# Performance work log

Hardware: AMD Instinct MI355X
Metric: run time of the kernel (lower is better)

Reference implementation:

```python
import jax, jax.numpy as jnp
import numpy as np

NUM_HEADS = 8
HEAD_DIM = 64
SCALE = HEAD_DIM ** -0.5
EPS = 1e-5
STRIDE = (2, 2)


def _layernorm(x, g, b):
    mu = x.mean(-1, keepdims=True)
    var = x.var(-1, keepdims=True)
    return (x - mu) * jax.lax.rsqrt(var + EPS) * g + b


def _pool(t, convw, ln_g, ln_b, H):
    # t: (B, T, nh, 1 + H*H, d); depthwise-conv pool of spatial tokens, cls kept as-is,
    # LayerNorm over per-head channel dim applied after re-attaching cls (matches torch).
    B, T, nh, N, d = t.shape
    t = t.reshape(B * T, nh, N, d)
    cls_tok, body = t[:, :, :1], t[:, :, 1:]
    xs = body.reshape(B * T * nh, H, H, d)
    xs = jax.lax.conv_general_dilated(
        xs, convw, window_strides=STRIDE, padding=((1, 1), (1, 1)),
        dimension_numbers=('NHWC', 'HWIO', 'NHWC'), feature_group_count=d)
    Ho, Wo = xs.shape[1], xs.shape[2]
    xs = xs.reshape(B * T, nh, Ho * Wo, d)
    xs = jnp.concatenate([cls_tok, xs], axis=2)
    xs = _layernorm(xs, ln_g, ln_b)
    return xs.reshape(B, T, nh, Ho * Wo + 1, d), (Ho, Wo)


def _lin(t, w, b):
    # (B, T, nh, n, d) -> fold heads -> Linear(nh*d -> nh*d) -> unfold heads
    B, T, nh, n, d = t.shape
    y = t.transpose(0, 1, 3, 2, 4).reshape(B * T, n, nh * d)
    y = y @ w.T + b
    return y.reshape(B, T, n, nh, d).transpose(0, 1, 3, 2, 4)


def reference(x, x_ref, w_q, b_q, w_k, b_k, w_v, b_v, w_proj, b_proj,
              convw_q, convw_k, convw_v, ln_g_q, ln_b_q, ln_g_k, ln_b_k,
              ln_g_v, ln_b_v, rel_pos_h, rel_pos_w, hw_shape):
    B, T1, N, C = x.shape
    T2 = x_ref.shape[1]
    nh, d = NUM_HEADS, C // NUM_HEADS
    H = int(hw_shape)
    # pool_first: split heads before pooling;  q from x, k = v from x_ref
    q = x.reshape(B, T1, N, nh, d).transpose(0, 1, 3, 2, 4)
    kv = x_ref.reshape(B, T2, N, nh, d).transpose(0, 1, 3, 2, 4)
    q, q_shape = _pool(q, convw_q, ln_g_q, ln_b_q, H)
    k, k_shape = _pool(kv, convw_k, ln_g_k, ln_b_k, H)
    v, _ = _pool(kv, convw_v, ln_g_v, ln_b_v, H)
    q = _lin(q, w_q, b_q)
    k = _lin(k, w_k, b_k)
    v = _lin(v, w_v, b_v)
    # b t nh n d -> b nh (t n) d
    q = q.transpose(0, 2, 1, 3, 4).reshape(B, nh, -1, d)
    k = k.transpose(0, 2, 1, 3, 4).reshape(B, nh, -1, d)
    v = v.transpose(0, 2, 1, 3, 4).reshape(B, nh, -1, d)
    attn = jnp.einsum('bhqd,bhkd->bhqk', q * SCALE, k)
    # inline spatial relative position bias (uses UNSCALED q, as in torch source)
    qh, qw = q_shape
    kh, kw = k_shape
    dh = (np.arange(qh)[:, None] * max(kh / qh, 1.0)
          - np.arange(kh)[None, :] * max(qh / kh, 1.0)
          + (kh - 1) * max(qh / kh, 1.0)).astype(np.int32)
    dw = (np.arange(qw)[:, None] * max(kw / qw, 1.0)
          - np.arange(kw)[None, :] * max(qw / kw, 1.0)
          + (kw - 1) * max(qw / kw, 1.0)).astype(np.int32)
    Rh = rel_pos_h[dh]  # (qh, kh, d)
    Rw = rel_pos_w[dw]  # (qw, kw, d)
    r_q = q[:, :, 1:].reshape(B, nh, qh, qw, d)
    rel_h = jnp.einsum('byhwc,hkc->byhwk', r_q, Rh)
    rel_w = jnp.einsum('byhwc,wkc->byhwk', r_q, Rw)
    bias = (rel_h[..., :, None] + rel_w[..., None, :]).reshape(B, nh, qh * qw, kh * kw)
    attn = attn.at[:, :, 1:, 1:].add(bias)
    attn = jax.nn.softmax(attn, axis=-1)
    out = jnp.einsum('bhqk,bhkd->bhqd', attn, v)
    # residual pooling (skips cls token)
    out = out.at[:, :, 1:, :].add(q[:, :, 1:, :])
    qN = out.shape[2]
    out = out.transpose(0, 2, 1, 3).reshape(B, qN, nh * d)
    out = out @ w_proj.T + b_proj
    return out.reshape(B, T1, qN // T1, nh * d)


def setup_inputs() -> dict:
    key = jax.random.key(0)
    ks = jax.random.split(key, 16)
    B, T, H, C = 8, 1, 56, 512
    nh, d = NUM_HEADS, HEAD_DIM
    N = H * H + 1
    rel_dim = 2 * (H // 2) - 1  # 55
    f32 = jnp.float32
    return {
        'x': jax.random.normal(ks[0], (B, T, N, C), f32),
        'x_ref': jax.random.normal(ks[1], (B, T, N, C), f32),
        'w_q': jax.random.normal(ks[2], (C, C), f32) * 0.02,
        'b_q': jnp.zeros((C,), f32),
        'w_k': jax.random.normal(ks[3], (C, C), f32) * 0.02,
        'b_k': jnp.zeros((C,), f32),
        'w_v': jax.random.normal(ks[4], (C, C), f32) * 0.02,
        'b_v': jnp.zeros((C,), f32),
        'w_proj': jax.random.normal(ks[5], (C, C), f32) * 0.02,
        'b_proj': jnp.zeros((C,), f32),
        'convw_q': jax.random.normal(ks[6], (3, 3, 1, d), f32) * 0.1,
        'convw_k': jax.random.normal(ks[7], (3, 3, 1, d), f32) * 0.1,
        'convw_v': jax.random.normal(ks[8], (3, 3, 1, d), f32) * 0.1,
        'ln_g_q': jnp.ones((d,), f32), 'ln_b_q': jnp.zeros((d,), f32),
        'ln_g_k': jnp.ones((d,), f32), 'ln_b_k': jnp.zeros((d,), f32),
        'ln_g_v': jnp.ones((d,), f32), 'ln_b_v': jnp.zeros((d,), f32),
        'rel_pos_h': jax.random.normal(ks[9], (rel_dim, d), f32) * 0.02,
        'rel_pos_w': jax.random.normal(ks[10], (rel_dim, d), f32) * 0.02,
        'hw_shape': 56,
    }
```

## Files before the change

kernel.cpp:

```cpp
#include <hip/hip_runtime.h>

#define NH    8
#define DH    64
#define NTOK  3137
#define NOUT  785
#define CDIM  512
#define ROWS  6280
#define HO    28
#define HIN   56
#define NKT   13
#define RELD  55
#define LOG2E 1.4426950408889634f

typedef unsigned short u16;
typedef __attribute__((ext_vector_type(8))) short bf16x8;
typedef __attribute__((ext_vector_type(4))) float f32x4;

__device__ __forceinline__ float b2f(u16 u) { return __uint_as_float(((unsigned)u) << 16); }
__device__ __forceinline__ u16 f2b(float f) {
  unsigned u = __float_as_uint(f);
  return (u16)((u + 0x7FFFu + ((u >> 16) & 1u)) >> 16);
}

__global__ __launch_bounds__(256) void pool_ln_kernel(
    const float* __restrict__ x, const float* __restrict__ xr,
    const float* __restrict__ cwq, const float* __restrict__ cwk, const float* __restrict__ cwv,
    const float* __restrict__ gq, const float* __restrict__ bq,
    const float* __restrict__ gk, const float* __restrict__ bk,
    const float* __restrict__ gv, const float* __restrict__ bv,
    u16* __restrict__ Pq, u16* __restrict__ Pk, u16* __restrict__ Pv)
{
  int tid   = threadIdx.x;
  int n     = blockIdx.x * 2 + (tid >> 7);
  int b     = blockIdx.y;
  int which = blockIdx.z;
  if (n >= NOUT) return;
  int c4 = tid & 127;
  int c  = c4 * 4;
  int d0 = c & 63;

  const float* src  = which ? xr : x;
  const float* srcb = src + (size_t)b * NTOK * CDIM + c;
  size_t obase = (size_t)(b * NOUT + n) * CDIM + c;

  float4 vq = make_float4(0.f, 0.f, 0.f, 0.f);
  float4 vk = make_float4(0.f, 0.f, 0.f, 0.f);
  const float* cw0 = which ? cwk : cwq;

  if (n == 0) {
    float4 t = *(const float4*)(srcb);
    vq = t; vk = t;
  } else {
    int oy = (n - 1) / HO, ox = (n - 1) % HO;
#pragma unroll
    for (int ky = 0; ky < 3; ++ky) {
      int iy = oy * 2 - 1 + ky;
      if (iy < 0 || iy >= HIN) continue;
#pragma unroll
      for (int kx = 0; kx < 3; ++kx) {
        int ix = ox * 2 - 1 + kx;
        if (ix < 0 || ix >= HIN) continue;
        int tok = 1 + iy * HIN + ix;
        float4 t  = *(const float4*)(srcb + (size_t)tok * CDIM);
        float4 w0 = *(const float4*)(cw0 + (ky * 3 + kx) * DH + d0);
        vq.x += t.x * w0.x; vq.y += t.y * w0.y; vq.z += t.z * w0.z; vq.w += t.w * w0.w;
        if (which) {
          float4 w1 = *(const float4*)(cwv + (ky * 3 + kx) * DH + d0);
          vk.x += t.x * w1.x; vk.y += t.y * w1.y; vk.z += t.z * w1.z; vk.w += t.w * w1.w;
        }
      }
    }
  }

  {
    float s  = vq.x + vq.y + vq.z + vq.w;
    float sq = vq.x * vq.x + vq.y * vq.y + vq.z * vq.z + vq.w * vq.w;
#pragma unroll
    for (int off = 1; off < 16; off <<= 1) {
      s  += __shfl_xor(s, off, 64);
      sq += __shfl_xor(sq, off, 64);
    }
    float mu  = s * (1.f / 64.f);
    float var = sq * (1.f / 64.f) - mu * mu;
    float inv = rsqrtf(var + 1e-5f);
    const float* g  = which ? gk : gq;
    const float* be = which ? bk : bq;
    float4 gg = *(const float4*)(g + d0);
    float4 bb = *(const float4*)(be + d0);
    ushort4 o;
    o.x = f2b((vq.x - mu) * inv * gg.x + bb.x);
    o.y = f2b((vq.y - mu) * inv * gg.y + bb.y);
    o.z = f2b((vq.z - mu) * inv * gg.z + bb.z);
    o.w = f2b((vq.w - mu) * inv * gg.w + bb.w);
    *(ushort4*)(((which ? Pk : Pq)) + obase) = o;
  }
  if (which) {
    float s  = vk.x + vk.y + vk.z + vk.w;
    float sq = vk.x * vk.x + vk.y * vk.y + vk.z * vk.z + vk.w * vk.w;
#pragma unroll
    for (int off = 1; off < 16; off <<= 1) {
      s  += __shfl_xor(s, off, 64);
      sq += __shfl_xor(sq, off, 64);
    }
    float mu  = s * (1.f / 64.f);
    float var = sq * (1.f / 64.f) - mu * mu;
    float inv = rsqrtf(var + 1e-5f);
    float4 gg = *(const float4*)(gv + d0);
    float4 bb = *(const float4*)(bv + d0);
    ushort4 o;
    o.x = f2b((vk.x - mu) * inv * gg.x + bb.x);
    o.y = f2b((vk.y - mu) * inv * gg.y + bb.y);
    o.z = f2b((vk.z - mu) * inv * gg.z + bb.z);
    o.w = f2b((vk.w - mu) * inv * gg.w + bb.w);
    *(ushort4*)(Pv + obase) = o;
  }
}

__global__ __launch_bounds__(256) void wcvt_kernel(
    const float* __restrict__ W0, const float* __restrict__ W1,
    const float* __restrict__ W2, const float* __restrict__ W3,
    u16* __restrict__ out)
{
  int idx = blockIdx.x * blockDim.x + threadIdx.x;
  const int per = CDIM * CDIM / 4;
  int mat = idx / per, off = (idx - mat * per) * 4;
  const float* src = (mat == 0) ? W0 : (mat == 1) ? W1 : (mat == 2) ? W2 : W3;
  float4 v = *(const float4*)(src + off);
  ushort4 o;
  o.x = f2b(v.x); o.y = f2b(v.y); o.z = f2b(v.z); o.w = f2b(v.w);
  *(ushort4*)(out + (size_t)mat * (CDIM * CDIM) + off) = o;
}

__global__ __launch_bounds__(256) void rcvt_kernel(
    const float* __restrict__ rph, const float* __restrict__ rpw,
    u16* __restrict__ Rhb, u16* __restrict__ Rwb)
{
  int idx = blockIdx.x * blockDim.x + threadIdx.x;
  if (idx >= 64 * 64) return;
  int r = idx >> 6, d = idx & 63;
  Rhb[idx] = (r < RELD) ? f2b(rph[r * DH + d] * LOG2E) : 0;
  Rwb[idx] = (r < RELD) ? f2b(rpw[r * DH + d] * LOG2E) : 0;
}

__global__ __launch_bounds__(256) void mgemm3_kernel(
    const u16* __restrict__ Xq, const u16* __restrict__ Xk, const u16* __restrict__ Xv,
    const u16* __restrict__ Wb, const float* __restrict__ bq,
    const float* __restrict__ bk, const float* __restrict__ bv,
    u16* __restrict__ Yq, u16* __restrict__ Yk, u16* __restrict__ Yv)
{
  int z = blockIdx.z;
  const u16* X = (z == 0) ? Xq : (z == 1) ? Xk : Xv;
  const u16* W = Wb + (size_t)z * CDIM * CDIM;
  const float* bias = (z == 0) ? bq : (z == 1) ? bk : bv;
  u16* Y = (z == 0) ? Yq : (z == 1) ? Yk : Yv;

  int tid = threadIdx.x;
  int w = tid >> 6, lane = tid & 63, l15 = lane & 15, lg = lane >> 4;
  int m0 = blockIdx.x * 64 + (w >> 1) * 32;
  int n0 = blockIdx.y * 128 + (w & 1) * 64;

  f32x4 acc[2][4] = {};
  float bs[4];
#pragma unroll
  for (int nf = 0; nf < 4; ++nf) bs[nf] = bias[n0 + nf * 16 + l15];

  for (int k0 = 0; k0 < CDIM; k0 += 32) {
    bf16x8 a[2], b[4];
#pragma unroll
    for (int mf = 0; mf < 2; ++mf) {
      int r = m0 + mf * 16 + l15;
      if (r > ROWS - 1) r = ROWS - 1;
      a[mf] = *(const bf16x8*)(X + (size_t)r * CDIM + k0 + lg * 8);
    }
#pragma unroll
    for (int nf = 0; nf < 4; ++nf) {
      int co = n0 + nf * 16 + l15;
      b[nf] = *(const bf16x8*)(W + (size_t)co * CDIM + k0 + lg * 8);
    }
#pragma unroll
    for (int mf = 0; mf < 2; ++mf)
#pragma unroll
      for (int nf = 0; nf < 4; ++nf)
        acc[mf][nf] = __builtin_amdgcn_mfma_f32_16x16x32_bf16(a[mf], b[nf], acc[mf][nf], 0, 0, 0);
  }

#pragma unroll
  for (int mf = 0; mf < 2; ++mf) {
#pragma unroll
    for (int j = 0; j < 4; ++j) {
      int r = m0 + mf * 16 + lg * 4 + j;
      if (r >= ROWS) continue;
      int bb = r / NOUT, n = r % NOUT;
#pragma unroll
      for (int nf = 0; nf < 4; ++nf) {
        int co = n0 + nf * 16 + l15;
        float v = acc[mf][nf][j] + bs[nf];
        Y[(((size_t)bb * NH + (co >> 6)) * NOUT + n) * DH + (co & 63)] = f2b(v);
      }
    }
  }
}

__global__ __launch_bounds__(256) void mgemm_proj_kernel(
    const u16* __restrict__ X, const u16* __restrict__ Wb, const float* __restrict__ bias,
    float* __restrict__ Y)
{
  int tid = threadIdx.x;
  int w = tid >> 6, lane = tid & 63, l15 = lane & 15, lg = lane >> 4;
  int m0 = blockIdx.x * 64 + (w >> 1) * 32;
  int n0 = blockIdx.y * 128 + (w & 1) * 64;

  f32x4 acc[2][4] = {};
  float bs[4];
#pragma unroll
  for (int nf = 0; nf < 4; ++nf) bs[nf] = bias[n0 + nf * 16 + l15];

  for (int k0 = 0; k0 < CDIM; k0 += 32) {
    bf16x8 a[2], b[4];
#pragma unroll
    for (int mf = 0; mf < 2; ++mf) {
      int r = m0 + mf * 16 + l15;
      if (r > ROWS - 1) r = ROWS - 1;
      a[mf] = *(const bf16x8*)(X + (size_t)r * CDIM + k0 + lg * 8);
    }
#pragma unroll
    for (int nf = 0; nf < 4; ++nf) {
      int co = n0 + nf * 16 + l15;
      b[nf] = *(const bf16x8*)(Wb + (size_t)co * CDIM + k0 + lg * 8);
    }
#pragma unroll
    for (int mf = 0; mf < 2; ++mf)
#pragma unroll
      for (int nf = 0; nf < 4; ++nf)
        acc[mf][nf] = __builtin_amdgcn_mfma_f32_16x16x32_bf16(a[mf], b[nf], acc[mf][nf], 0, 0, 0);
  }

#pragma unroll
  for (int mf = 0; mf < 2; ++mf) {
#pragma unroll
    for (int j = 0; j < 4; ++j) {
      int r = m0 + mf * 16 + lg * 4 + j;
      if (r >= ROWS) continue;
#pragma unroll
      for (int nf = 0; nf < 4; ++nf) {
        int co = n0 + nf * 16 + l15;
        Y[(size_t)r * CDIM + co] = acc[mf][nf][j] + bs[nf];
      }
    }
  }
}

__global__ __launch_bounds__(256, 4) void fattn_kernel(
    const u16* __restrict__ Q, const u16* __restrict__ K, const u16* __restrict__ V,
    const u16* __restrict__ Rhb, const u16* __restrict__ Rwb,
    u16* __restrict__ O)
{
  __shared__ u16 Vs[2][64][64];
  __shared__ u16 Ps[4][16][72];
  __shared__ u16 relh[64][RELD];
  __shared__ u16 relw[64][RELD];

  int bid = blockIdx.x;
  int nbid = (bid & 7) * 104 + (bid >> 3);
  int bh = nbid / NKT, qt = nbid % NKT;

  int tid = threadIdx.x;
  int w = tid >> 6, lane = tid & 63, l15 = lane & 15, lg = lane >> 4;
  size_t base = (size_t)bh * NOUT * DH;
  int q0 = qt * 64;

  int vkey_l = tid & 63;
  int vd0 = (tid >> 6) * 16;

  int qrow_qi = min(q0 + w * 16 + l15, NOUT - 1);
  const u16* qp = Q + base + (size_t)qrow_qi * DH + lg * 8;
  bf16x8 qa0 = *(const bf16x8*)(qp);
  bf16x8 qa1 = *(const bf16x8*)(qp + 32);

  {
    int key = min(vkey_l, NOUT - 1);
    const u16* vp = V + base + (size_t)key * DH + vd0;
    bf16x8 v0 = *(const bf16x8*)(vp);
    bf16x8 v1 = *(const bf16x8*)(vp + 8);
#pragma unroll
    for (int i = 0; i < 8; ++i) {
      int d = vd0 + i;
      Vs[0][d][((((vkey_l >> 3) ^ (d & 7)) << 3) | (vkey_l & 7))] = (u16)v0[i];
    }
#pragma unroll
    for (int i = 0; i < 8; ++i) {
      int d = vd0 + 8 + i;
      Vs[0][d][((((vkey_l >> 3) ^ (d & 7)) << 3) | (vkey_l & 7))] = (u16)v1[i];
    }
  }

#pragma unroll
  for (int nf = 0; nf < 4; ++nf) {
    int rr = nf * 16 + l15;
    const u16* hp = Rhb + rr * 64 + lg * 8;
    bf16x8 hb0 = *(const bf16x8*)(hp);
    bf16x8 hb1 = *(const bf16x8*)(hp + 32);
    f32x4 ah = {};
    ah = __builtin_amdgcn_mfma_f32_16x16x32_bf16(qa0, hb0, ah, 0, 0, 0);
    ah = __builtin_amdgcn_mfma_f32_16x16x32_bf16(qa1, hb1, ah, 0, 0, 0);
    const u16* wp = Rwb + rr * 64 + lg * 8;
    bf16x8 wb0 = *(const bf16x8*)(wp);
    bf16x8 wb1 = *(const bf16x8*)(wp + 32);
    f32x4 aw = {};
    aw = __builtin_amdgcn_mfma_f32_16x16x32_bf16(qa0, wb0, aw, 0, 0, 0);
    aw = __builtin_amdgcn_mfma_f32_16x16x32_bf16(qa1, wb1, aw, 0, 0, 0);
    if (rr < RELD) {
#pragma unroll
      for (int j = 0; j < 4; ++j) {
        relh[w * 16 + lg * 4 + j][rr] = f2b(ah[j]);
        relw[w * 16 + lg * 4 + j][rr] = f2b(aw[j]);
      }
    }
  }

  int qy_j[4], qx_j[4];
  bool qv_j[4];
#pragma unroll
  for (int j = 0; j < 4; ++j) {
    int qi = q0 + w * 16 + lg * 4 + j;
    qv_j[j] = (qi >= 1);
    int qm1 = qi - 1;
    qy_j[j] = qm1 / HO;
    qx_j[j] = qm1 % HO;
  }

  int kyr[4], kxr[4];
#pragma unroll
  for (int sub = 0; sub < 4; ++sub) {
    int km1 = sub * 16 + l15 - 1;
    kyr[sub] = km1 / HO;
    kxr[sub] = km1 % HO;
  }

  f32x4 o0 = {}, o1 = {}, o2 = {}, o3 = {};
  float mrow[4], lrow[4];
#pragma unroll
  for (int j = 0; j < 4; ++j) { mrow[j] = -1e30f; lrow[j] = 0.f; }

  const float QKSCALE = 0.125f * LOG2E;

  for (int t = 0; t < NKT; ++t) {
    int k0 = t * 64;
    int cur = t & 1;
    __syncthreads();

    bf16x8 nv0, nv1;
    bool have_next = (t + 1 < NKT);
    if (have_next) {
      int key = min(k0 + 64 + vkey_l, NOUT - 1);
      const u16* vp = V + base + (size_t)key * DH + vd0;
      nv0 = *(const bf16x8*)(vp);
      nv1 = *(const bf16x8*)(vp + 8);
    }

    bf16x8 kb[4][2];
#pragma unroll
    for (int sub = 0; sub < 4; ++sub) {
      int key = k0 + sub * 16 + l15;
      int keff = min(key, NOUT - 1);
      const u16* kp = K + base + (size_t)keff * DH + lg * 8;
      kb[sub][0] = *(const bf16x8*)(kp);
      kb[sub][1] = *(const bf16x8*)(kp + 32);
    }

    f32x4 s[4];
#pragma unroll
    for (int sub = 0; sub < 4; ++sub) {
      int key = k0 + sub * 16 + l15;
      f32x4 acc = {};
      acc = __builtin_amdgcn_mfma_f32_16x16x32_bf16(qa0, kb[sub][0], acc, 0, 0, 0);
      acc = __builtin_amdgcn_mfma_f32_16x16x32_bf16(qa1, kb[sub][1], acc, 0, 0, 0);
      bool kv = key < NOUT;
      int ky = kyr[sub], kx = kxr[sub];
#pragma unroll
      for (int j = 0; j < 4; ++j) {
        float v = acc[j] * QKSCALE;
        if (key >= 1 && kv && qv_j[j]) {
          int ql = w * 16 + lg * 4 + j;
          v += b2f(relh[ql][qy_j[j] - ky + 27]) + b2f(relw[ql][qx_j[j] - kx + 27]);
        }
        if (!kv) v = -1e30f;
        s[sub][j] = v;
      }
    }

#pragma unroll
    for (int sub = 0; sub < 4; ++sub) {
      kxr[sub] += 8; kyr[sub] += 2;
      if (kxr[sub] >= HO) { kxr[sub] -= HO; kyr[sub] += 1; }
    }

    if (have_next) {
#pragma unroll
      for (int i = 0; i < 8; ++i) {
        int d = vd0 + i;
        Vs[cur ^ 1][d][((((vkey_l >> 3) ^ (d & 7)) << 3) | (vkey_l & 7))] = (u16)nv0[i];
      }
#pragma unroll
      for (int i = 0; i < 8; ++i) {
        int d = vd0 + 8 + i;
        Vs[cur ^ 1][d][((((vkey_l >> 3) ^ (d & 7)) << 3) | (vkey_l & 7))] = (u16)nv1[i];
      }
    }

#pragma unroll
    for (int j = 0; j < 4; ++j) {
      float lm = fmaxf(fmaxf(s[0][j], s[1][j]), fmaxf(s[2][j], s[3][j]));
      lm = fmaxf(lm, __shfl_xor(lm, 1));
      lm = fmaxf(lm, __shfl_xor(lm, 2));
      lm = fmaxf(lm, __shfl_xor(lm, 4));
      lm = fmaxf(lm, __shfl_xor(lm, 8));
      if (lm > mrow[j]) {
        float a = exp2f(mrow[j] - lm);
        mrow[j] = lm;
        o0[j] *= a; o1[j] *= a; o2[j] *= a; o3[j] *= a;
        lrow[j] *= a;
      }
      float ps = 0.f;
#pragma unroll
      for (int sub = 0; sub < 4; ++sub) {
        float pv = exp2f(s[sub][j] - mrow[j]);
        s[sub][j] = pv;
        ps += pv;
      }
      lrow[j] += ps;
    }

#pragma unroll
    for (int j = 0; j < 4; ++j) {
      Ps[w][lg * 4 + j][ 0 + l15] = f2b(s[0][j]);
      Ps[w][lg * 4 + j][16 + l15] = f2b(s[1][j]);
      Ps[w][lg * 4 + j][32 + l15] = f2b(s[2][j]);
      Ps[w][lg * 4 + j][48 + l15] = f2b(s[3][j]);
    }

    bf16x8 pa0 = *(const bf16x8*)&Ps[w][l15][lg * 8];
    bf16x8 pa1 = *(const bf16x8*)&Ps[w][l15][32 + lg * 8];
    {
      int r = 0 + l15;
      bf16x8 vb0 = *(const bf16x8*)&Vs[cur][r][((lg ^ (r & 7)) << 3)];
      bf16x8 vb1 = *(const bf16x8*)&Vs[cur][r][(((4 + lg) ^ (r & 7)) << 3)];
      o0 = __builtin_amdgcn_mfma_f32_16x16x32_bf16(pa0, vb0, o0, 0, 0, 0);
      o0 = __builtin_amdgcn_mfma_f32_16x16x32_bf16(pa1, vb1, o0, 0, 0, 0);
    }
    {
      int r = 16 + l15;
      bf16x8 vb0 = *(const bf16x8*)&Vs[cur][r][((lg ^ (r & 7)) << 3)];
      bf16x8 vb1 = *(const bf16x8*)&Vs[cur][r][(((4 + lg) ^ (r & 7)) << 3)];
      o1 = __builtin_amdgcn_mfma_f32_16x16x32_bf16(pa0, vb0, o1, 0, 0, 0);
      o1 = __builtin_amdgcn_mfma_f32_16x16x32_bf16(pa1, vb1, o1, 0, 0, 0);
    }
    {
      int r = 32 + l15;
      bf16x8 vb0 = *(const bf16x8*)&Vs[cur][r][((lg ^ (r & 7)) << 3)];
      bf16x8 vb1 = *(const bf16x8*)&Vs[cur][r][(((4 + lg) ^ (r & 7)) << 3)];
      o2 = __builtin_amdgcn_mfma_f32_16x16x32_bf16(pa0, vb0, o2, 0, 0, 0);
      o2 = __builtin_amdgcn_mfma_f32_16x16x32_bf16(pa1, vb1, o2, 0, 0, 0);
    }
    {
      int r = 48 + l15;
      bf16x8 vb0 = *(const bf16x8*)&Vs[cur][r][((lg ^ (r & 7)) << 3)];
      bf16x8 vb1 = *(const bf16x8*)&Vs[cur][r][(((4 + lg) ^ (r & 7)) << 3)];
      o3 = __builtin_amdgcn_mfma_f32_16x16x32_bf16(pa0, vb0, o3, 0, 0, 0);
      o3 = __builtin_amdgcn_mfma_f32_16x16x32_bf16(pa1, vb1, o3, 0, 0, 0);
    }
  }

  int b = bh >> 3, h = bh & 7;
#pragma unroll
  for (int j = 0; j < 4; ++j) {
    int ql = w * 16 + lg * 4 + j;
    int qi = q0 + ql;
    float l = lrow[j];
    l += __shfl_xor(l, 1);
    l += __shfl_xor(l, 2);
    l += __shfl_xor(l, 4);
    l += __shfl_xor(l, 8);
    if (qi >= NOUT) continue;
    float inv = 1.f / l;
    float v0 = o0[j] * inv, v1 = o1[j] * inv, v2 = o2[j] * inv, v3 = o3[j] * inv;
    if (qi > 0) {
      const u16* qp2 = Q + base + (size_t)qi * DH;
      v0 += b2f(qp2[ 0 + l15]);
      v1 += b2f(qp2[16 + l15]);
      v2 += b2f(qp2[32 + l15]);
      v3 += b2f(qp2[48 + l15]);
    }
    size_t ob = ((size_t)b * NOUT + qi) * CDIM + h * DH;
    O[ob +  0 + l15] = f2b(v0);
    O[ob + 16 + l15] = f2b(v1);
    O[ob + 32 + l15] = f2b(v2);
    O[ob + 48 + l15] = f2b(v3);
  }
}

extern "C" void kernel_launch(void* const* d_in, const int* in_sizes, int n_in,
                              void* d_out, int out_size, void* d_ws, size_t ws_size,
                              hipStream_t stream) {
  const float* x     = (const float*)d_in[0];
  const float* xr    = (const float*)d_in[1];
  const float* wq    = (const float*)d_in[2];
  const float* bq    = (const float*)d_in[3];
  const float* wk    = (const float*)d_in[4];
  const float* bk    = (const float*)d_in[5];
  const float* wv    = (const float*)d_in[6];
  const float* bv    = (const float*)d_in[7];
  const float* wpj   = (const float*)d_in[8];
  const float* bpj   = (const float*)d_in[9];
  const float* cwq   = (const float*)d_in[10];
  const float* cwk   = (const float*)d_in[11];
  const float* cwv   = (const float*)d_in[12];
  const float* gq    = (const float*)d_in[13];
  const float* lbq   = (const float*)d_in[14];
  const float* gk    = (const float*)d_in[15];
  const float* lbk   = (const float*)d_in[16];
  const float* gv    = (const float*)d_in[17];
  const float* lbv   = (const float*)d_in[18];
  const float* rph   = (const float*)d_in[19];
  const float* rpw   = (const float*)d_in[20];
  (void)in_sizes; (void)n_in; (void)out_size; (void)ws_size;

  u16* ws = (u16*)d_ws;
  const size_t PSZ = (size_t)ROWS * CDIM;
  const size_t WSZ = (size_t)CDIM * CDIM;
  u16* s0 = ws + 0 * PSZ;
  u16* s1 = ws + 1 * PSZ;
  u16* s2 = ws + 2 * PSZ;
  u16* s3 = ws + 3 * PSZ;
  u16* s4 = ws + 4 * PSZ;
  u16* Wb  = ws + 5 * PSZ;
  u16* Rhb = Wb + 4 * WSZ;
  u16* Rwb = Rhb + 64 * 64;
  u16* qbuf = (u16*)d_out;

  pool_ln_kernel<<<dim3((NOUT + 1) / 2, 8, 2), 256, 0, stream>>>(
      x, xr, cwq, cwk, cwv, gq, lbq, gk, lbk, gv, lbv, s0, s1, s2);

  wcvt_kernel<<<(4 * CDIM * CDIM / 4 + 255) / 256, 256, 0, stream>>>(wq, wk, wv, wpj, Wb);
  rcvt_kernel<<<16, 256, 0, stream>>>(rph, rpw, Rhb, Rwb);

  dim3 g3((ROWS + 63) / 64, CDIM / 128, 3);
  mgemm3_kernel<<<g3, 256, 0, stream>>>(s0, s1, s2, Wb, bq, bk, bv, qbuf, s3, s4);

  fattn_kernel<<<NKT * 64, 256, 0, stream>>>(qbuf, s3, s4, Rhb, Rwb, s0);

  dim3 gp((ROWS + 63) / 64, CDIM / 128);
  mgemm_proj_kernel<<<gp, 256, 0, stream>>>(s0, Wb + 3 * WSZ, bpj, (float*)d_out);
}
```

Measured before the change: 197.3 us.

## Pack V LDS stores as pairs, reorder V prefetch, and prioritize MFMA blocks

Each thread now loads two adjacent V keys and writes them into the transposed LDS tile as packed 32-bit stores, halving the number of LDS store instructions. The next-tile V global loads are issued after the K loads, and their LDS stores move after the softmax. The QK and PV MFMA groups are separated from surrounding ALU/LDS work and wrapped in s_setprio to favour matrix issue across waves. This rearranges the schedule of the attention loop and may change register pressure and the bank-conflict behaviour of the swizzled stores.

```diff
diff --git a/kernel.cpp b/kernel.cpp
--- a/kernel.cpp
+++ b/kernel.cpp
@@ -13,12 +13,13 @@
 #define LOG2E 1.4426950408889634f
 
 typedef unsigned short u16;
+typedef unsigned int u32;
 typedef __attribute__((ext_vector_type(8))) short bf16x8;
 typedef __attribute__((ext_vector_type(4))) float f32x4;
 
-__device__ __forceinline__ float b2f(u16 u) { return __uint_as_float(((unsigned)u) << 16); }
+__device__ __forceinline__ float b2f(u16 u) { return __uint_as_float(((u32)u) << 16); }
 __device__ __forceinline__ u16 f2b(float f) {
-  unsigned u = __float_as_uint(f);
+  u32 u = __float_as_uint(f);
   return (u16)((u + 0x7FFFu + ((u >> 16) & 1u)) >> 16);
 }
 
@@ -269,8 +270,8 @@
   size_t base = (size_t)bh * NOUT * DH;
   int q0 = qt * 64;
 
-  int vkey_l = tid & 63;
-  int vd0 = (tid >> 6) * 16;
+  int vkp = (tid & 31) * 2;
+  int vdb = (tid >> 5) * 8;
 
   int qrow_qi = min(q0 + w * 16 + l15, NOUT - 1);
   const u16* qp = Q + base + (size_t)qrow_qi * DH + lg * 8;
@@ -278,19 +279,15 @@
   bf16x8 qa1 = *(const bf16x8*)(qp + 32);
 
   {
-    int key = min(vkey_l, NOUT - 1);
-    const u16* vp = V + base + (size_t)key * DH + vd0;
-    bf16x8 v0 = *(const bf16x8*)(vp);
-    bf16x8 v1 = *(const bf16x8*)(vp + 8);
+    int ke = min(vkp, NOUT - 1), ko = min(vkp + 1, NOUT - 1);
+    bf16x8 ve = *(const bf16x8*)(V + base + (size_t)ke * DH + vdb);
+    bf16x8 vo = *(const bf16x8*)(V + base + (size_t)ko * DH + vdb);
 #pragma unroll
     for (int i = 0; i < 8; ++i) {
-      int d = vd0 + i;
-      Vs[0][d][((((vkey_l >> 3) ^ (d & 7)) << 3) | (vkey_l & 7))] = (u16)v0[i];
-    }
-#pragma unroll
-    for (int i = 0; i < 8; ++i) {
-      int d = vd0 + 8 + i;
-      Vs[0][d][((((vkey_l >> 3) ^ (d & 7)) << 3) | (vkey_l & 7))] = (u16)v1[i];
+      int d = vdb + i;
+      int col = ((((vkp >> 3) ^ (d & 7)) << 3) | (vkp & 7));
+      u32 pk = (u32)(u16)ve[i] | ((u32)(u16)vo[i] << 16);
+      *(u32*)&Vs[0][d][col] = pk;
     }
   }
 
@@ -349,15 +346,6 @@
     int cur = t & 1;
     __syncthreads();
 
-    bf16x8 nv0, nv1;
-    bool have_next = (t + 1 < NKT);
-    if (have_next) {
-      int key = min(k0 + 64 + vkey_l, NOUT - 1);
-      const u16* vp = V + base + (size_t)key * DH + vd0;
-      nv0 = *(const bf16x8*)(vp);
-      nv1 = *(const bf16x8*)(vp + 8);
-    }
-
     bf16x8 kb[4][2];
 #pragma unroll
     for (int sub = 0; sub < 4; ++sub) {
@@ -368,18 +356,32 @@
       kb[sub][1] = *(const bf16x8*)(kp + 32);
     }
 
+    bf16x8 nve, nvo;
+    bool have_next = (t + 1 < NKT);
+    if (have_next) {
+      int ke = min(k0 + 64 + vkp, NOUT - 1), ko = min(k0 + 64 + vkp + 1, NOUT - 1);
+      nve = *(const bf16x8*)(V + base + (size_t)ke * DH + vdb);
+      nvo = *(const bf16x8*)(V + base + (size_t)ko * DH + vdb);
+    }
+
     f32x4 s[4];
+    __builtin_amdgcn_s_setprio(1);
 #pragma unroll
     for (int sub = 0; sub < 4; ++sub) {
-      int key = k0 + sub * 16 + l15;
       f32x4 acc = {};
       acc = __builtin_amdgcn_mfma_f32_16x16x32_bf16(qa0, kb[sub][0], acc, 0, 0, 0);
       acc = __builtin_amdgcn_mfma_f32_16x16x32_bf16(qa1, kb[sub][1], acc, 0, 0, 0);
+      s[sub] = acc;
+    }
+    __builtin_amdgcn_s_setprio(0);
+#pragma unroll
+    for (int sub = 0; sub < 4; ++sub) {
+      int key = k0 + sub * 16 + l15;
       bool kv = key < NOUT;
       int ky = kyr[sub], kx = kxr[sub];
 #pragma unroll
       for (int j = 0; j < 4; ++j) {
-        float v = acc[j] * QKSCALE;
+        float v = s[sub][j] * QKSCALE;
         if (key >= 1 && kv && qv_j[j]) {
           int ql = w * 16 + lg * 4 + j;
           v += b2f(relh[ql][qy_j[j] - ky + 27]) + b2f(relw[ql][qx_j[j] - kx + 27]);
@@ -393,19 +395,6 @@
     for (int sub = 0; sub < 4; ++sub) {
       kxr[sub] += 8; kyr[sub] += 2;
       if (kxr[sub] >= HO) { kxr[sub] -= HO; kyr[sub] += 1; }
-    }
-
-    if (have_next) {
-#pragma unroll
-      for (int i = 0; i < 8; ++i) {
-        int d = vd0 + i;
-        Vs[cur ^ 1][d][((((vkey_l >> 3) ^ (d & 7)) << 3) | (vkey_l & 7))] = (u16)nv0[i];
-      }
-#pragma unroll
-      for (int i = 0; i < 8; ++i) {
-        int d = vd0 + 8 + i;
-        Vs[cur ^ 1][d][((((vkey_l >> 3) ^ (d & 7)) << 3) | (vkey_l & 7))] = (u16)nv1[i];
-      }
     }
 
 #pragma unroll
@@ -431,6 +420,16 @@
       lrow[j] += ps;
     }
 
+    if (have_next) {
+#pragma unroll
+      for (int i = 0; i < 8; ++i) {
+        int d = vdb + i;
+        int col = ((((vkp >> 3) ^ (d & 7)) << 3) | (vkp & 7));
+        u32 pk = (u32)(u16)nve[i] | ((u32)(u16)nvo[i] << 16);
+        *(u32*)&Vs[cur ^ 1][d][col] = pk;
+      }
+    }
+
 #pragma unroll
     for (int j = 0; j < 4; ++j) {
       Ps[w][lg * 4 + j][ 0 + l15] = f2b(s[0][j]);
@@ -441,34 +440,37 @@
 
     bf16x8 pa0 = *(const bf16x8*)&Ps[w][l15][lg * 8];
     bf16x8 pa1 = *(const bf16x8*)&Ps[w][l15][32 + lg * 8];
+    bf16x8 vb00, vb01, vb10, vb11, vb20, vb21, vb30, vb31;
     {
       int r = 0 + l15;
-      bf16x8 vb0 = *(const bf16x8*)&Vs[cur][r][((lg ^ (r & 7)) << 3)];
-      bf16x8 vb1 = *(const bf16x8*)&Vs[cur][r][(((4 + lg) ^ (r & 7)) << 3)];
-      o0 = __builtin_amdgcn_mfma_f32_16x16x32_bf16(pa0, vb0, o0, 0, 0, 0);
-      o0 = __builtin_amdgcn_mfma_f32_16x16x32_bf16(pa1, vb1, o0, 0, 0, 0);
+      vb00 = *(const bf16x8*)&Vs[cur][r][((lg ^ (r & 7)) << 3)];
+      vb01 = *(const bf16x8*)&Vs[cur][r][(((4 + lg) ^ (r & 7)) << 3)];
     }
     {
       int r = 16 + l15;
-      bf16x8 vb0 = *(const bf16x8*)&Vs[cur][r][((lg ^ (r & 7)) << 3)];
-      bf16x8 vb1 = *(const bf16x8*)&Vs[cur][r][(((4 + lg) ^ (r & 7)) << 3)];
-      o1 = __builtin_amdgcn_mfma_f32_16x16x32_bf16(pa0, vb0, o1, 0, 0, 0);
-      o1 = __builtin_amdgcn_mfma_f32_16x16x32_bf16(pa1, vb1, o1, 0, 0, 0);
+      vb10 = *(const bf16x8*)&Vs[cur][r][((lg ^ (r & 7)) << 3)];
+      vb11 = *(const bf16x8*)&Vs[cur][r][(((4 + lg) ^ (r & 7)) << 3)];
     }
     {
       int r = 32 + l15;
-      bf16x8 vb0 = *(const bf16x8*)&Vs[cur][r][((lg ^ (r & 7)) << 3)];
-      bf16x8 vb1 = *(const bf16x8*)&Vs[cur][r][(((4 + lg) ^ (r & 7)) << 3)];
-      o2 = __builtin_amdgcn_mfma_f32_16x16x32_bf16(pa0, vb0, o2, 0, 0, 0);
-      o2 = __builtin_amdgcn_mfma_f32_16x16x32_bf16(pa1, vb1, o2, 0, 0, 0);
+      vb20 = *(const bf16x8*)&Vs[cur][r][((lg ^ (r & 7)) << 3)];
+      vb21 = *(const bf16x8*)&Vs[cur][r][(((4 + lg) ^ (r & 7)) << 3)];
     }
     {
       int r = 48 + l15;
-      bf16x8 vb0 = *(const bf16x8*)&Vs[cur][r][((lg ^ (r & 7)) << 3)];
-      bf16x8 vb1 = *(const bf16x8*)&Vs[cur][r][(((4 + lg) ^ (r & 7)) << 3)];
-      o3 = __builtin_amdgcn_mfma_f32_16x16x32_bf16(pa0, vb0, o3, 0, 0, 0);
-      o3 = __builtin_amdgcn_mfma_f32_16x16x32_bf16(pa1, vb1, o3, 0, 0, 0);
-    }
+      vb30 = *(const bf16x8*)&Vs[cur][r][((lg ^ (r & 7)) << 3)];
+      vb31 = *(const bf16x8*)&Vs[cur][r][(((4 + lg) ^ (r & 7)) << 3)];
+    }
+    __builtin_amdgcn_s_setprio(1);
+    o0 = __builtin_amdgcn_mfma_f32_16x16x32_bf16(pa0, vb00, o0, 0, 0, 0);
+    o0 = __builtin_amdgcn_mfma_f32_16x16x32_bf16(pa1, vb01, o0, 0, 0, 0);
+    o1 = __builtin_amdgcn_mfma_f32_16x16x32_bf16(pa0, vb10, o1, 0, 0, 0);
+    o1 = __builtin_amdgcn_mfma_f32_16x16x32_bf16(pa1, vb11, o1, 0, 0, 0);
+    o2 = __builtin_amdgcn_mfma_f32_16x16x32_bf16(pa0, vb20, o2, 0, 0, 0);
+    o2 = __builtin_amdgcn_mfma_f32_16x16x32_bf16(pa1, vb21, o2, 0, 0, 0);
+    o3 = __builtin_amdgcn_mfma_f32_16x16x32_bf16(pa0, vb30, o3, 0, 0, 0);
+    o3 = __builtin_amdgcn_mfma_f32_16x16x32_bf16(pa1, vb31, o3, 0, 0, 0);
+    __builtin_amdgcn_s_setprio(0);
   }
 
   int b = bh >> 3, h = bh & 7;
```

Result: no change. 199.1 us (median of 2 runs) (+1.0%).
